# Kernel optimization log

Hardware: AMD Instinct MI355X
Metric: run time of the kernel (lower is better)

Reference implementation:

```python
import jax, jax.numpy as jnp
import numpy as np

N_NODES = 50000
N_EDGES = 800000
N_GRAPHS = 256
NEG_SLOPE = 0.2

def selu(x):
    return jax.nn.selu(x)

def gat_conv(x, src, dst, W, att_l, att_r, b, n_nodes):
    """PyG GATConv, heads=1, with self-loops already appended to (src, dst).
    Message j->i: alpha_ij = softmax_i(leaky_relu(a_l.h_j + a_r.h_i)); out_i = sum_j alpha_ij h_j + b."""
    h = x @ W                                   # [N, C]
    a_src = h @ att_l                           # [N]
    a_dst = h @ att_r                           # [N]
    e = jax.nn.leaky_relu(a_src[src] + a_dst[dst], NEG_SLOPE)   # [E]
    # segment softmax over incoming edges of each dst node
    m = jax.ops.segment_max(e, dst, num_segments=n_nodes)       # [N]
    m = jnp.where(jnp.isfinite(m), m, 0.0)
    ex = jnp.exp(e - m[dst])
    denom = jax.ops.segment_sum(ex, dst, num_segments=n_nodes)  # [N]
    alpha = ex / jnp.maximum(denom, 1e-16)[dst]                  # [E]
    out = jax.ops.segment_sum(h[src] * alpha[:, None], dst, num_segments=n_nodes)
    return out + b

def global_mean_pool(x, batch, n_graphs):
    s = jax.ops.segment_sum(x, batch, num_segments=n_graphs)
    cnt = jax.ops.segment_sum(jnp.ones((x.shape[0],), x.dtype), batch, num_segments=n_graphs)
    return s / jnp.maximum(cnt, 1.0)[:, None]

def setup_inputs() -> dict:
    key = jax.random.key(0)
    ks = jax.random.split(key, 12)
    F_in, C, H, NC = 310, 256, 128, 2
    x = jax.random.normal(ks[0], (N_NODES, F_in), dtype=jnp.float32)
    edge_index = jax.random.randint(ks[1], (2, N_EDGES), 0, N_NODES, dtype=jnp.int64)
    batch = jnp.sort(jax.random.randint(ks[2], (N_NODES,), 0, N_GRAPHS, dtype=jnp.int64))
    g = lambda k, shp: jax.random.normal(k, shp, dtype=jnp.float32) * 0.05
    return {
        "x": x, "edge_index": edge_index, "batch": batch,
        "W1": g(ks[3], (F_in, C)), "att_l1": g(ks[4], (C,)), "att_r1": g(ks[5], (C,)),
        "b1": jnp.zeros((C,), jnp.float32),
        "W2": g(ks[6], (C, C)), "att_l2": g(ks[7], (C,)), "att_r2": g(ks[8], (C,)),
        "b2": jnp.zeros((C,), jnp.float32),
        "fc1_W": g(ks[9], (C, H)), "fc1_b": jnp.zeros((H,), jnp.float32),
        "fc2_W": g(ks[10], (H, NC)), "fc2_b": jnp.zeros((NC,), jnp.float32),
    }

def reference(x, edge_index, batch, W1, att_l1, att_r1, b1, W2, att_l2, att_r2, b2,
              fc1_W, fc1_b, fc2_W, fc2_b):
    n = x.shape[0]
    loops = jnp.arange(n, dtype=edge_index.dtype)
    src = jnp.concatenate([edge_index[0], loops])   # add_self_loops=True (PyG default)
    dst = jnp.concatenate([edge_index[1], loops])
    h = selu(gat_conv(x, src, dst, W1, att_l1, att_r1, b1, n))
    h = selu(gat_conv(h, src, dst, W2, att_l2, att_r2, b2, n))
    g = selu(global_mean_pool(h, batch, N_GRAPHS))      # [G, 256]
    g = selu(g @ fc1_W + fc1_b)                         # [G, 128]
    # dropout is identity in eval mode
    return jax.nn.log_softmax(g @ fc2_W + fc2_b, axis=-1)  # [G, 2]
```

## Files before the change

### kernel.cpp

```cpp
#include <hip/hip_runtime.h>
#include <hip/hip_bf16.h>

#define N_NODES 50000
#define N_EDGES 800000
#define N_TOT   (N_EDGES + N_NODES)
#define N_GRAPHS 256
#define F_IN 310
#define KP1 320
#define CH 256
#define HID 128
#define DEG_CAP 128

typedef __attribute__((ext_vector_type(8))) short short8;
typedef __attribute__((ext_vector_type(4))) float f32x4;
typedef unsigned short ushort_t;

__device__ __forceinline__ float selu_f(float x) {
    const float scale = 1.0507009873554805f;
    const float alpha = 1.6732632423543772f;
    return x > 0.f ? scale * x : scale * alpha * (expm1f(x));
}

__device__ __forceinline__ ushort_t f32_to_bf16_rne(float f) {
    unsigned u = __float_as_uint(f);
    unsigned rounding = 0x7FFFu + ((u >> 16) & 1u);
    return (ushort_t)((u + rounding) >> 16);
}
__device__ __forceinline__ float bf16_to_f32(ushort_t v) {
    return __uint_as_float(((unsigned)v) << 16);
}

__global__ __launch_bounds__(256) void convert_wt_both(
        const float* __restrict__ W1, ushort_t* __restrict__ W1t,
        const float* __restrict__ W2, ushort_t* __restrict__ W2t) {
    int i = blockIdx.x * blockDim.x + threadIdx.x;
    const int n1 = CH * KP1;
    if (i < n1) {
        int n = i / KP1, k = i % KP1;
        W1t[i] = (k < F_IN) ? f32_to_bf16_rne(W1[(long)k * CH + n]) : 0;
    } else {
        int j = i - n1;
        if (j >= CH * CH) return;
        int n = j / CH, k = j % CH;
        W2t[j] = f32_to_bf16_rne(W2[(long)k * CH + n]);
    }
}

template<int AF32>
__global__ __launch_bounds__(256) void gemm_bf16_fused_t(
        const void* __restrict__ Asrc, const ushort_t* __restrict__ Bt,
        ushort_t* __restrict__ Cb, const float* __restrict__ att_l,
        const float* __restrict__ att_r, float* __restrict__ a_srcv,
        float* __restrict__ a_dstv, int M, int Kp) {
    __shared__ __align__(16) ushort_t As[2][64 * 32];
    __shared__ __align__(16) ushort_t Bs[2][256 * 32];
    __shared__ float s_pl[64], s_pr[64];
    int tid = threadIdx.x;
    int row0 = blockIdx.x * 64;
    int w = tid >> 6, l = tid & 63;
    int lr = l & 15, lc = l >> 4;
    f32x4 acc[4][4] = {};

    int srow = l >> 2;
    int sc = l & 3;
    int sx = sc ^ (srow & 3);
    int garow = row0 + w * 16 + srow; if (garow >= M) garow = M - 1;
    const ushort_t* gB[4];
#pragma unroll
    for (int g = 0; g < 4; ++g)
        gB[g] = Bt + (size_t)(w * 64 + g * 16 + srow) * Kp + sx * 8;
    int nt = Kp >> 5;

    const ushort_t* gA = nullptr;
    const float* xrow = nullptr;
    if (AF32) xrow = (const float*)Asrc + (size_t)garow * F_IN;
    else      gA = (const ushort_t*)Asrc + (size_t)garow * Kp + sx * 8;

    auto stageB = [&](int sel, int k0) {
#pragma unroll
        for (int g = 0; g < 4; ++g)
            __builtin_amdgcn_global_load_lds(
                (const __attribute__((address_space(1))) void*)(gB[g] + k0),
                (__attribute__((address_space(3))) void*)(&Bs[sel][(w * 64 + g * 16) * 32]), 16, 0, 0);
    };
    auto stageA_glds = [&](int sel, int k0) {
        __builtin_amdgcn_global_load_lds(
            (const __attribute__((address_space(1))) void*)(gA + k0),
            (__attribute__((address_space(3))) void*)(&As[sel][w * 16 * 32]), 16, 0, 0);
    };
    float va[8];
    auto loadA_f32 = [&](int k0) {
        int kc = k0 + sc * 8;
        if (kc + 8 <= F_IN) {
#pragma unroll
            for (int j = 0; j < 4; ++j) {
                float2 p = *(const float2*)(xrow + kc + j * 2);
                va[j * 2] = p.x; va[j * 2 + 1] = p.y;
            }
        } else {
#pragma unroll
            for (int j = 0; j < 8; ++j)
                va[j] = (kc + j < F_IN) ? xrow[kc + j] : 0.f;
        }
    };
    auto writeA = [&](int sel) {
        short8 s;
#pragma unroll
        for (int j = 0; j < 8; ++j) s[j] = (short)f32_to_bf16_rne(va[j]);
        *(short8*)(&As[sel][(w * 16 + srow) * 32 + sx * 8]) = s;
    };

    if (AF32) loadA_f32(0); else stageA_glds(0, 0);
    stageB(0, 0);
    if (AF32) writeA(0);
    __syncthreads();
    int cur = 0;
    for (int t = 0; t < nt; ++t) {
        int k1 = (t + 1) << 5;
        if (t + 1 < nt) {
            if (AF32) loadA_f32(k1); else stageA_glds(cur ^ 1, k1);
            stageB(cur ^ 1, k1);
        }
        short8 af[4], bfv[4];
#pragma unroll
        for (int mi = 0; mi < 4; ++mi) {
            int r = mi * 16 + lr;
            af[mi] = *(const short8*)(&As[cur][r * 32 + ((lc ^ (r & 3)) * 8)]);
        }
#pragma unroll
        for (int ni = 0; ni < 4; ++ni) {
            int r = w * 64 + ni * 16 + lr;
            bfv[ni] = *(const short8*)(&Bs[cur][r * 32 + ((lc ^ (r & 3)) * 8)]);
        }
#pragma unroll
        for (int mi = 0; mi < 4; ++mi)
#pragma unroll
            for (int ni = 0; ni < 4; ++ni)
                acc[mi][ni] = __builtin_amdgcn_mfma_f32_16x16x32_bf16(
                    af[mi], bfv[ni], acc[mi][ni], 0, 0, 0);
        if (AF32 && t + 1 < nt) writeA(cur ^ 1);
        __syncthreads();
        cur ^= 1;
    }

    if (tid < 64) { s_pl[tid] = 0.f; s_pr[tid] = 0.f; }
    __syncthreads();
    float al[4], ar[4];
#pragma unroll
    for (int ni = 0; ni < 4; ++ni) {
        int col = w * 64 + ni * 16 + lr;
        al[ni] = att_l[col];
        ar[ni] = att_r[col];
    }
#pragma unroll
    for (int mi = 0; mi < 4; ++mi) {
        int lrow = mi * 16 + lc * 4;
#pragma unroll
        for (int q = 0; q < 4; ++q) {
            int grow = row0 + lrow + q;
            float pl = 0.f, pr = 0.f;
#pragma unroll
            for (int ni = 0; ni < 4; ++ni) {
                float v = acc[mi][ni][q];
                pl += v * al[ni];
                pr += v * ar[ni];
                if (grow < M)
                    Cb[(size_t)grow * CH + w * 64 + ni * 16 + lr] = f32_to_bf16_rne(v);
            }
#pragma unroll
            for (int off = 1; off < 16; off <<= 1) {
                pl += __shfl_xor(pl, off);
                pr += __shfl_xor(pr, off);
            }
            if (lr == 0) {
                atomicAdd(&s_pl[lrow + q], pl);
                atomicAdd(&s_pr[lrow + q], pr);
            }
        }
    }
    __syncthreads();
    if (tid < 64 && row0 + tid < M) {
        a_srcv[row0 + tid] = s_pl[tid];
        a_dstv[row0 + tid] = s_pr[tid];
    }
}

__global__ __launch_bounds__(256) void deg_count(
        const int* __restrict__ ei, int* __restrict__ deg) {
    int eid = blockIdx.x * blockDim.x + threadIdx.x;
    if (eid >= N_TOT) return;
    int d = (eid < N_EDGES) ? ei[N_EDGES + eid] : eid - N_EDGES;
    atomicAdd(&deg[d], 1);
}

__global__ __launch_bounds__(256) void reserve_k(
        const int* __restrict__ deg, int* __restrict__ start,
        int* __restrict__ fillpos, int* __restrict__ cursor, int n) {
    int i = blockIdx.x * blockDim.x + threadIdx.x;
    if (i >= n) return;
    int s = atomicAdd(cursor, deg[i]);
    start[i] = s;
    fillpos[i] = s;
}

__global__ __launch_bounds__(256) void csr_fill(
        const int* __restrict__ ei, int* __restrict__ fillpos,
        int* __restrict__ csr_src) {
    int eid = blockIdx.x * blockDim.x + threadIdx.x;
    if (eid >= N_TOT) return;
    int s, d;
    if (eid < N_EDGES) { s = ei[eid]; d = ei[N_EDGES + eid]; }
    else { s = eid - N_EDGES; d = s; }
    int p = atomicAdd(&fillpos[d], 1);
    csr_src[p] = s;
}

__global__ __launch_bounds__(256) void gat_aggregate(
        const int* __restrict__ start, const int* __restrict__ deg,
        const int* __restrict__ csr_src,
        const float* __restrict__ a_src, const float* __restrict__ a_dst,
        const ushort_t* __restrict__ h, const float* __restrict__ bias,
        ushort_t* __restrict__ out_bf, int n) {
    __shared__ int   s_idx[4][DEG_CAP];
    __shared__ float s_ex[4][DEG_CAP];
    int wid = threadIdx.x >> 6;
    int lane = threadIdx.x & 63;
    int node = blockIdx.x * 4 + wid;
    if (node >= n) return;
    int s0 = start[node];
    int dg = deg[node];
    float ad = a_dst[node];
    bool cached = (dg <= DEG_CAP);

    float sum = 0.f;
    for (int i = lane; i < dg; i += 64) {
        int s = csr_src[s0 + i];
        float e = a_src[s] + ad;
        e = fmaxf(e, 0.2f * e);
        float ex = __expf(e);
        if (cached) { s_idx[wid][i] = s; s_ex[wid][i] = ex; }
        sum += ex;
    }
#pragma unroll
    for (int off = 32; off > 0; off >>= 1) sum += __shfl_xor(sum, off);
    float inv = 1.f / fmaxf(sum, 1e-16f);

    float4 acc = {0.f, 0.f, 0.f, 0.f};
    if (cached) {
        int i = 0;
        for (; i + 8 <= dg; i += 8) {
            int   si[8];
            float xi[8];
            ushort4 hv[8];
#pragma unroll
            for (int j = 0; j < 8; ++j) {
                si[j] = s_idx[wid][i + j];
                xi[j] = s_ex[wid][i + j] * inv;
            }
#pragma unroll
            for (int j = 0; j < 8; ++j)
                hv[j] = *(const ushort4*)(h + (long)si[j] * CH + lane * 4);
#pragma unroll
            for (int j = 0; j < 8; ++j) {
                acc.x += xi[j] * bf16_to_f32(hv[j].x);
                acc.y += xi[j] * bf16_to_f32(hv[j].y);
                acc.z += xi[j] * bf16_to_f32(hv[j].z);
                acc.w += xi[j] * bf16_to_f32(hv[j].w);
            }
        }
        for (; i + 4 <= dg; i += 4) {
            int sa = s_idx[wid][i],     sb = s_idx[wid][i + 1];
            int sc_ = s_idx[wid][i + 2], sd = s_idx[wid][i + 3];
            float xa = s_ex[wid][i] * inv,     xb = s_ex[wid][i + 1] * inv;
            float xc = s_ex[wid][i + 2] * inv, xd = s_ex[wid][i + 3] * inv;
            ushort4 ha = *(const ushort4*)(h + (long)sa * CH + lane * 4);
            ushort4 hb = *(const ushort4*)(h + (long)sb * CH + lane * 4);
            ushort4 hc = *(const ushort4*)(h + (long)sc_ * CH + lane * 4);
            ushort4 hd = *(const ushort4*)(h + (long)sd * CH + lane * 4);
            acc.x += xa * bf16_to_f32(ha.x) + xb * bf16_to_f32(hb.x)
                   + xc * bf16_to_f32(hc.x) + xd * bf16_to_f32(hd.x);
            acc.y += xa * bf16_to_f32(ha.y) + xb * bf16_to_f32(hb.y)
                   + xc * bf16_to_f32(hc.y) + xd * bf16_to_f32(hd.y);
            acc.z += xa * bf16_to_f32(ha.z) + xb * bf16_to_f32(hb.z)
                   + xc * bf16_to_f32(hc.z) + xd * bf16_to_f32(hd.z);
            acc.w += xa * bf16_to_f32(ha.w) + xb * bf16_to_f32(hb.w)
                   + xc * bf16_to_f32(hc.w) + xd * bf16_to_f32(hd.w);
        }
        for (; i < dg; i++) {
            int s = s_idx[wid][i];
            float xa = s_ex[wid][i] * inv;
            ushort4 hv = *(const ushort4*)(h + (long)s * CH + lane * 4);
            acc.x += xa * bf16_to_f32(hv.x);
            acc.y += xa * bf16_to_f32(hv.y);
            acc.z += xa * bf16_to_f32(hv.z);
            acc.w += xa * bf16_to_f32(hv.w);
        }
    } else {
        for (int i = 0; i < dg; i++) {
            int s = csr_src[s0 + i];
            float e = a_src[s] + ad;
            e = fmaxf(e, 0.2f * e);
            float alpha = __expf(e) * inv;
            ushort4 hv = *(const ushort4*)(h + (long)s * CH + lane * 4);
            acc.x += alpha * bf16_to_f32(hv.x);
            acc.y += alpha * bf16_to_f32(hv.y);
            acc.z += alpha * bf16_to_f32(hv.z);
            acc.w += alpha * bf16_to_f32(hv.w);
        }
    }
    float4 bv = *(const float4*)(bias + lane * 4);
    ushort4 ob;
    ob.x = f32_to_bf16_rne(selu_f(acc.x + bv.x));
    ob.y = f32_to_bf16_rne(selu_f(acc.y + bv.y));
    ob.z = f32_to_bf16_rne(selu_f(acc.z + bv.z));
    ob.w = f32_to_bf16_rne(selu_f(acc.w + bv.w));
    *(ushort4*)(out_bf + (long)node * CH + lane * 4) = ob;
}

__global__ __launch_bounds__(1024) void pool_head_kernel(
        const ushort_t* __restrict__ h, const int* __restrict__ batch,
        const float* __restrict__ fc1W, const float* __restrict__ fc1b,
        const float* __restrict__ fc2W, const float* __restrict__ fc2b,
        float* __restrict__ out) {
    __shared__ float part[4][CH];
    __shared__ float row[CH];
    __shared__ float part2[8][HID];
    __shared__ float hrow[HID];
    __shared__ float logits[2];
    int g = blockIdx.x;
    int tid = threadIdx.x;
    int t = tid & 255;
    int quad = tid >> 8;
    int lo, hi;
    { int a = 0, b = N_NODES;
      while (a < b) { int mid = (a + b) >> 1; if (batch[mid] < g) a = mid + 1; else b = mid; }
      lo = a; }
    { int a = lo, b = N_NODES;
      while (a < b) { int mid = (a + b) >> 1; if (batch[mid] < g + 1) a = mid + 1; else b = mid; }
      hi = a; }
    float a0 = 0.f, a1 = 0.f;
    int i = lo + quad;
    for (; i + 4 < hi; i += 8) {
        a0 += bf16_to_f32(h[(long)i * CH + t]);
        a1 += bf16_to_f32(h[(long)(i + 4) * CH + t]);
    }
    for (; i < hi; i += 4) a0 += bf16_to_f32(h[(long)i * CH + t]);
    part[quad][t] = a0 + a1;
    __syncthreads();
    if (quad == 0) {
        float cnt = (float)(hi - lo);
        float acc = (part[0][t] + part[1][t]) + (part[2][t] + part[3][t]);
        row[t] = selu_f(acc / fmaxf(cnt, 1.f));
    }
    __syncthreads();
    {
        int o = tid & 127;
        int seg = tid >> 7;
        float s = 0.f;
        int k0 = seg * 32;
        for (int k = k0; k < k0 + 32; ++k) s += row[k] * fc1W[k * HID + o];
        part2[seg][o] = s;
    }
    __syncthreads();
    if (tid < HID) {
        float s = fc1b[tid];
#pragma unroll
        for (int j = 0; j < 8; ++j) s += part2[j][tid];
        hrow[tid] = selu_f(s);
    }
    __syncthreads();
    if (tid < 2) {
        float a = fc2b[tid];
        for (int k = 0; k < HID; k++) a += hrow[k] * fc2W[k * 2 + tid];
        logits[tid] = a;
    }
    __syncthreads();
    if (tid < 2) {
        float m = fmaxf(logits[0], logits[1]);
        float lse = logf(expf(logits[0] - m) + expf(logits[1] - m)) + m;
        out[g * 2 + tid] = logits[tid] - lse;
    }
}

extern "C" void kernel_launch(void* const* d_in, const int* in_sizes, int n_in,
                              void* d_out, int out_size, void* d_ws, size_t ws_size,
                              hipStream_t stream) {
    const float* x      = (const float*)d_in[0];
    const int*   ei     = (const int*)d_in[1];
    const int*   batch  = (const int*)d_in[2];
    const float* W1     = (const float*)d_in[3];
    const float* att_l1 = (const float*)d_in[4];
    const float* att_r1 = (const float*)d_in[5];
    const float* b1     = (const float*)d_in[6];
    const float* W2     = (const float*)d_in[7];
    const float* att_l2 = (const float*)d_in[8];
    const float* att_r2 = (const float*)d_in[9];
    const float* b2     = (const float*)d_in[10];
    const float* fc1W   = (const float*)d_in[11];
    const float* fc1b   = (const float*)d_in[12];
    const float* fc2W   = (const float*)d_in[13];
    const float* fc2b   = (const float*)d_in[14];
    float* out = (float*)d_out;

    char* ws = (char*)d_ws;
    size_t off = 0;
    auto alloc = [&](size_t bytes) {
        void* p = ws + off;
        off += (bytes + 255) & ~(size_t)255;
        return p;
    };
    ushort_t* Hb1    = (ushort_t*)alloc((size_t)N_NODES * CH * 2);
    ushort_t* Zb2    = (ushort_t*)alloc((size_t)N_NODES * CH * 2);
    ushort_t* Hb2    = (ushort_t*)alloc((size_t)N_NODES * CH * 2);
    ushort_t* W1t    = (ushort_t*)alloc((size_t)CH * KP1 * 2);
    ushort_t* W2t    = (ushort_t*)alloc((size_t)CH * CH * 2);
    float*    a_src  = (float*)alloc((size_t)N_NODES * 4);
    float*    a_dst  = (float*)alloc((size_t)N_NODES * 4);
    int*      deg    = (int*)alloc((size_t)N_NODES * 4);
    int*      cursor = (int*)alloc(256);
    int*      startA = (int*)alloc((size_t)N_NODES * 4);
    int*      fillpos= (int*)alloc((size_t)N_NODES * 4);
    int*      csr_src= (int*)alloc((size_t)N_TOT * 4);

    size_t deg_pad = ((size_t)N_NODES * 4 + 255) & ~(size_t)255;

    dim3 blk(256);
    int gemm_grid = (N_NODES + 63) / 64;
    int wt_grid   = (CH * KP1 + CH * CH + 255) / 256;
    int edge_grid = (N_TOT + 255) / 256;
    int node_grid = (N_NODES + 255) / 256;
    int agg_grid  = (N_NODES + 3) / 4;

    convert_wt_both<<<wt_grid, blk, 0, stream>>>(W1, W1t, W2, W2t);
    hipMemsetAsync(deg, 0, deg_pad + 4, stream);
    deg_count<<<edge_grid, blk, 0, stream>>>(ei, deg);
    reserve_k<<<node_grid, blk, 0, stream>>>(deg, startA, fillpos, cursor, N_NODES);
    csr_fill<<<edge_grid, blk, 0, stream>>>(ei, fillpos, csr_src);

    gemm_bf16_fused_t<1><<<gemm_grid, blk, 0, stream>>>(x, W1t, Hb1, att_l1, att_r1,
                                                        a_src, a_dst, N_NODES, KP1);
    gat_aggregate<<<agg_grid, blk, 0, stream>>>(startA, deg, csr_src, a_src, a_dst,
                                                Hb1, b1, Zb2, N_NODES);

    gemm_bf16_fused_t<0><<<gemm_grid, blk, 0, stream>>>(Zb2, W2t, Hb2, att_l2, att_r2,
                                                        a_src, a_dst, N_NODES, CH);
    gat_aggregate<<<agg_grid, blk, 0, stream>>>(startA, deg, csr_src, a_src, a_dst,
                                                Hb2, b2, Hb1, N_NODES);

    pool_head_kernel<<<N_GRAPHS, dim3(1024), 0, stream>>>(Hb1, batch, fc1W, fc1b,
                                                          fc2W, fc2b, out);
}
```

Baseline: 323.4 us.

## Single-pass GAT aggregation with shuffles, fuse weight convert with degree count

Merges the weight-transpose/convert kernel and the degree-count kernel into one launch by splitting the grid by block index. Rewrites the aggregation so that one pass over each 64-edge chunk computes the exp weights and broadcasts source indices and weights with wave shuffles instead of shared memory. Normalisation by the softmax sum is deferred to the end. This removes the second edge pass, the shared arrays and the high-degree fallback path. The GEMM also reuses the A tile's shared memory for the attention partial sums and gets a launch-bounds occupancy hint, trading some register headroom for occupancy.

```diff
diff --git a/kernel.cpp b/kernel.cpp
--- a/kernel.cpp
+++ b/kernel.cpp
@@ -9,7 +9,6 @@
 #define KP1 320
 #define CH 256
 #define HID 128
-#define DEG_CAP 128
 
 typedef __attribute__((ext_vector_type(8))) short short8;
 typedef __attribute__((ext_vector_type(4))) float f32x4;
@@ -30,31 +29,40 @@
     return __uint_as_float(((unsigned)v) << 16);
 }
 
-__global__ __launch_bounds__(256) void convert_wt_both(
+#define WT_BLKS ((CH * KP1 + CH * CH + 255) / 256)
+__global__ __launch_bounds__(256) void convert_wt_deg(
         const float* __restrict__ W1, ushort_t* __restrict__ W1t,
-        const float* __restrict__ W2, ushort_t* __restrict__ W2t) {
-    int i = blockIdx.x * blockDim.x + threadIdx.x;
-    const int n1 = CH * KP1;
-    if (i < n1) {
-        int n = i / KP1, k = i % KP1;
-        W1t[i] = (k < F_IN) ? f32_to_bf16_rne(W1[(long)k * CH + n]) : 0;
+        const float* __restrict__ W2, ushort_t* __restrict__ W2t,
+        const int* __restrict__ ei, int* __restrict__ deg) {
+    int b = blockIdx.x;
+    if (b < WT_BLKS) {
+        int i = b * 256 + threadIdx.x;
+        const int n1 = CH * KP1;
+        if (i < n1) {
+            int n = i / KP1, k = i % KP1;
+            W1t[i] = (k < F_IN) ? f32_to_bf16_rne(W1[(long)k * CH + n]) : 0;
+        } else {
+            int j = i - n1;
+            if (j >= CH * CH) return;
+            int n = j / CH, k = j % CH;
+            W2t[j] = f32_to_bf16_rne(W2[(long)k * CH + n]);
+        }
     } else {
-        int j = i - n1;
-        if (j >= CH * CH) return;
-        int n = j / CH, k = j % CH;
-        W2t[j] = f32_to_bf16_rne(W2[(long)k * CH + n]);
+        int eid = (b - WT_BLKS) * 256 + threadIdx.x;
+        if (eid >= N_TOT) return;
+        int d = (eid < N_EDGES) ? ei[N_EDGES + eid] : eid - N_EDGES;
+        atomicAdd(&deg[d], 1);
     }
 }
 
 template<int AF32>
-__global__ __launch_bounds__(256) void gemm_bf16_fused_t(
+__global__ __launch_bounds__(256, 4) void gemm_bf16_fused_t(
         const void* __restrict__ Asrc, const ushort_t* __restrict__ Bt,
         ushort_t* __restrict__ Cb, const float* __restrict__ att_l,
         const float* __restrict__ att_r, float* __restrict__ a_srcv,
         float* __restrict__ a_dstv, int M, int Kp) {
     __shared__ __align__(16) ushort_t As[2][64 * 32];
     __shared__ __align__(16) ushort_t Bs[2][256 * 32];
-    __shared__ float s_pl[64], s_pr[64];
     int tid = threadIdx.x;
     int row0 = blockIdx.x * 64;
     int w = tid >> 6, l = tid & 63;
@@ -143,7 +151,9 @@
         cur ^= 1;
     }
 
-    if (tid < 64) { s_pl[tid] = 0.f; s_pr[tid] = 0.f; }
+    float* s_pl = (float*)&As[0][0];
+    float* s_pr = s_pl + 64;
+    if (tid < 128) s_pl[tid] = 0.f;
     __syncthreads();
     float al[4], ar[4];
 #pragma unroll
@@ -183,14 +193,6 @@
         a_srcv[row0 + tid] = s_pl[tid];
         a_dstv[row0 + tid] = s_pr[tid];
     }
-}
-
-__global__ __launch_bounds__(256) void deg_count(
-        const int* __restrict__ ei, int* __restrict__ deg) {
-    int eid = blockIdx.x * blockDim.x + threadIdx.x;
-    if (eid >= N_TOT) return;
-    int d = (eid < N_EDGES) ? ei[N_EDGES + eid] : eid - N_EDGES;
-    atomicAdd(&deg[d], 1);
 }
 
 __global__ __launch_bounds__(256) void reserve_k(
@@ -221,8 +223,6 @@
         const float* __restrict__ a_src, const float* __restrict__ a_dst,
         const ushort_t* __restrict__ h, const float* __restrict__ bias,
         ushort_t* __restrict__ out_bf, int n) {
-    __shared__ int   s_idx[4][DEG_CAP];
-    __shared__ float s_ex[4][DEG_CAP];
     int wid = threadIdx.x >> 6;
     int lane = threadIdx.x & 63;
     int node = blockIdx.x * 4 + wid;
@@ -230,90 +230,59 @@
     int s0 = start[node];
     int dg = deg[node];
     float ad = a_dst[node];
-    bool cached = (dg <= DEG_CAP);
-
-    float sum = 0.f;
-    for (int i = lane; i < dg; i += 64) {
-        int s = csr_src[s0 + i];
-        float e = a_src[s] + ad;
-        e = fmaxf(e, 0.2f * e);
-        float ex = __expf(e);
-        if (cached) { s_idx[wid][i] = s; s_ex[wid][i] = ex; }
-        sum += ex;
-    }
+
+    float sum_l = 0.f;
+    float4 acc = {0.f, 0.f, 0.f, 0.f};
+    for (int c = 0; c < dg; c += 64) {
+        int nc = min(64, dg - c);
+        int s_l = 0; float ex_l = 0.f;
+        if (lane < nc) {
+            s_l = csr_src[s0 + c + lane];
+            float e = a_src[s_l] + ad;
+            e = fmaxf(e, 0.2f * e);
+            ex_l = __expf(e);
+            sum_l += ex_l;
+        }
+        int j = 0;
+        for (; j + 8 <= nc; j += 8) {
+            int si[8]; float xi[8]; ushort4 hv[8];
+#pragma unroll
+            for (int k = 0; k < 8; ++k) {
+                si[k] = __shfl(s_l, j + k);
+                xi[k] = __shfl(ex_l, j + k);
+            }
+#pragma unroll
+            for (int k = 0; k < 8; ++k)
+                hv[k] = *(const ushort4*)(h + (long)si[k] * CH + lane * 4);
+#pragma unroll
+            for (int k = 0; k < 8; ++k) {
+                acc.x += xi[k] * bf16_to_f32(hv[k].x);
+                acc.y += xi[k] * bf16_to_f32(hv[k].y);
+                acc.z += xi[k] * bf16_to_f32(hv[k].z);
+                acc.w += xi[k] * bf16_to_f32(hv[k].w);
+            }
+        }
+        for (; j < nc; ++j) {
+            int sj = __shfl(s_l, j);
+            float xj = __shfl(ex_l, j);
+            ushort4 hv = *(const ushort4*)(h + (long)sj * CH + lane * 4);
+            acc.x += xj * bf16_to_f32(hv.x);
+            acc.y += xj * bf16_to_f32(hv.y);
+            acc.z += xj * bf16_to_f32(hv.z);
+            acc.w += xj * bf16_to_f32(hv.w);
+        }
+    }
+    float sum = sum_l;
 #pragma unroll
     for (int off = 32; off > 0; off >>= 1) sum += __shfl_xor(sum, off);
     float inv = 1.f / fmaxf(sum, 1e-16f);
 
-    float4 acc = {0.f, 0.f, 0.f, 0.f};
-    if (cached) {
-        int i = 0;
-        for (; i + 8 <= dg; i += 8) {
-            int   si[8];
-            float xi[8];
-            ushort4 hv[8];
-#pragma unroll
-            for (int j = 0; j < 8; ++j) {
-                si[j] = s_idx[wid][i + j];
-                xi[j] = s_ex[wid][i + j] * inv;
-            }
-#pragma unroll
-            for (int j = 0; j < 8; ++j)
-                hv[j] = *(const ushort4*)(h + (long)si[j] * CH + lane * 4);
-#pragma unroll
-            for (int j = 0; j < 8; ++j) {
-                acc.x += xi[j] * bf16_to_f32(hv[j].x);
-                acc.y += xi[j] * bf16_to_f32(hv[j].y);
-                acc.z += xi[j] * bf16_to_f32(hv[j].z);
-                acc.w += xi[j] * bf16_to_f32(hv[j].w);
-            }
-        }
-        for (; i + 4 <= dg; i += 4) {
-            int sa = s_idx[wid][i],     sb = s_idx[wid][i + 1];
-            int sc_ = s_idx[wid][i + 2], sd = s_idx[wid][i + 3];
-            float xa = s_ex[wid][i] * inv,     xb = s_ex[wid][i + 1] * inv;
-            float xc = s_ex[wid][i + 2] * inv, xd = s_ex[wid][i + 3] * inv;
-            ushort4 ha = *(const ushort4*)(h + (long)sa * CH + lane * 4);
-            ushort4 hb = *(const ushort4*)(h + (long)sb * CH + lane * 4);
-            ushort4 hc = *(const ushort4*)(h + (long)sc_ * CH + lane * 4);
-            ushort4 hd = *(const ushort4*)(h + (long)sd * CH + lane * 4);
-            acc.x += xa * bf16_to_f32(ha.x) + xb * bf16_to_f32(hb.x)
-                   + xc * bf16_to_f32(hc.x) + xd * bf16_to_f32(hd.x);
-            acc.y += xa * bf16_to_f32(ha.y) + xb * bf16_to_f32(hb.y)
-                   + xc * bf16_to_f32(hc.y) + xd * bf16_to_f32(hd.y);
-            acc.z += xa * bf16_to_f32(ha.z) + xb * bf16_to_f32(hb.z)
-                   + xc * bf16_to_f32(hc.z) + xd * bf16_to_f32(hd.z);
-            acc.w += xa * bf16_to_f32(ha.w) + xb * bf16_to_f32(hb.w)
-                   + xc * bf16_to_f32(hc.w) + xd * bf16_to_f32(hd.w);
-        }
-        for (; i < dg; i++) {
-            int s = s_idx[wid][i];
-            float xa = s_ex[wid][i] * inv;
-            ushort4 hv = *(const ushort4*)(h + (long)s * CH + lane * 4);
-            acc.x += xa * bf16_to_f32(hv.x);
-            acc.y += xa * bf16_to_f32(hv.y);
-            acc.z += xa * bf16_to_f32(hv.z);
-            acc.w += xa * bf16_to_f32(hv.w);
-        }
-    } else {
-        for (int i = 0; i < dg; i++) {
-            int s = csr_src[s0 + i];
-            float e = a_src[s] + ad;
-            e = fmaxf(e, 0.2f * e);
-            float alpha = __expf(e) * inv;
-            ushort4 hv = *(const ushort4*)(h + (long)s * CH + lane * 4);
-            acc.x += alpha * bf16_to_f32(hv.x);
-            acc.y += alpha * bf16_to_f32(hv.y);
-            acc.z += alpha * bf16_to_f32(hv.z);
-            acc.w += alpha * bf16_to_f32(hv.w);
-        }
-    }
     float4 bv = *(const float4*)(bias + lane * 4);
     ushort4 ob;
-    ob.x = f32_to_bf16_rne(selu_f(acc.x + bv.x));
-    ob.y = f32_to_bf16_rne(selu_f(acc.y + bv.y));
-    ob.z = f32_to_bf16_rne(selu_f(acc.z + bv.z));
-    ob.w = f32_to_bf16_rne(selu_f(acc.w + bv.w));
+    ob.x = f32_to_bf16_rne(selu_f(acc.x * inv + bv.x));
+    ob.y = f32_to_bf16_rne(selu_f(acc.y * inv + bv.y));
+    ob.z = f32_to_bf16_rne(selu_f(acc.z * inv + bv.z));
+    ob.w = f32_to_bf16_rne(selu_f(acc.w * inv + bv.w));
     *(ushort4*)(out_bf + (long)node * CH + lane * 4) = ob;
 }
 
@@ -426,14 +395,13 @@
 
     dim3 blk(256);
     int gemm_grid = (N_NODES + 63) / 64;
-    int wt_grid   = (CH * KP1 + CH * CH + 255) / 256;
     int edge_grid = (N_TOT + 255) / 256;
     int node_grid = (N_NODES + 255) / 256;
     int agg_grid  = (N_NODES + 3) / 4;
-
-    convert_wt_both<<<wt_grid, blk, 0, stream>>>(W1, W1t, W2, W2t);
+    int wtdeg_grid = WT_BLKS + edge_grid;
+
     hipMemsetAsync(deg, 0, deg_pad + 4, stream);
-    deg_count<<<edge_grid, blk, 0, stream>>>(ei, deg);
+    convert_wt_deg<<<wtdeg_grid, blk, 0, stream>>>(W1, W1t, W2, W2t, ei, deg);
     reserve_k<<<node_grid, blk, 0, stream>>>(deg, startA, fillpos, cursor, N_NODES);
     csr_fill<<<edge_grid, blk, 0, stream>>>(ei, fillpos, csr_src);
 
```

Result: faster. 313.5 us (-3.0%).
